# Optimization experiments

Hardware: AMD Instinct MI355X
Metric: run time of the kernel (lower is better)

Reference implementation:

```python
import jax, jax.numpy as jnp
import numpy as np

B, N, C, NSAMPLE = 4, 1024, 512, 32
RADIUS, HMIN, HMAX = 0.05, -0.02, 0.04
EPS = 1e-5


def setup_inputs() -> dict:
    key = jax.random.key(0)
    ks = jax.random.split(key, 6)
    # points in a ~20cm cube so the 5cm cylinder actually captures neighbors
    seed_xyz_graspable = jax.random.uniform(ks[0], (B, N, 3), jnp.float32) * 0.2
    seed_features_graspable = jax.random.normal(ks[1], (B, C, N), jnp.float32)
    rot_raw = jax.random.normal(ks[2], (B, N, 3, 3), jnp.float32)
    vp_rot, _ = jnp.linalg.qr(rot_raw)  # proper-ish per-seed view rotations
    W1 = jax.random.normal(ks[3], (512, 3 + C), jnp.float32) / np.float32(np.sqrt(3 + C))
    g1 = jnp.ones((512,), jnp.float32)
    b1 = jnp.zeros((512,), jnp.float32)
    W2 = jax.random.normal(ks[4], (512, 512), jnp.float32) / np.float32(np.sqrt(512))
    g2 = jnp.ones((512,), jnp.float32)
    b2 = jnp.zeros((512,), jnp.float32)
    return dict(seed_xyz_graspable=seed_xyz_graspable,
                seed_features_graspable=seed_features_graspable,
                vp_rot=vp_rot, W1=W1, g1=g1, b1=b1, W2=W2, g2=g2, b2=b2)


def _cylinder_query(xyz, rot):
    # offsets d[b,m,n] = xyz[b,n] - query[b,m], rotated into the cylinder frame (d @ R)
    d = xyz[:, None, :, :] - xyz[:, :, None, :]                 # (B,M,N,3)
    r = jnp.einsum('bmnd,bmde->bmne', d, rot)                   # (B,M,N,3)
    mask = (r[..., 1] ** 2 + r[..., 2] ** 2 < RADIUS ** 2) \
         & (r[..., 0] > HMIN) & (r[..., 0] < HMAX)              # (B,M,N)
    # first NSAMPLE valid indices; pad with the first valid index (CUDA kernel semantics)
    cand = jnp.where(mask, jnp.arange(N, dtype=jnp.int32)[None, None, :], N)
    idx = jnp.sort(cand, axis=-1)[..., :NSAMPLE]                # (B,M,S)
    idx = jnp.where(idx == N, idx[..., :1], idx)
    return idx


def _bn_relu(x, g, b):
    # training-mode BatchNorm2d over (B, M, S) per output channel; x: (B,O,M,S)
    mean = jnp.mean(x, axis=(0, 2, 3), keepdims=True)
    var = jnp.var(x, axis=(0, 2, 3), keepdims=True)
    xn = (x - mean) * jax.lax.rsqrt(var + EPS)
    return jax.nn.relu(xn * g[None, :, None, None] + b[None, :, None, None])


def reference(seed_xyz_graspable, seed_features_graspable, vp_rot, W1, g1, b1, W2, g2, b2):
    xyz = seed_xyz_graspable                                    # (B,N,3)
    idx = _cylinder_query(xyz, vp_rot)                          # (B,M,S) int32
    # gather neighbor coordinates and center/rotate/normalize
    grouped_xyz = jnp.take_along_axis(xyz[:, None], idx[..., None], axis=2)   # (B,M,S,3)
    local = grouped_xyz - xyz[:, :, None, :]
    local = jnp.einsum('bmsd,bmde->bmse', local, vp_rot) / RADIUS             # normalize_xyz
    # gather neighbor features
    feats = jnp.swapaxes(seed_features_graspable, 1, 2)                       # (B,N,C)
    gfeat = jnp.take_along_axis(feats[:, None], idx[..., None], axis=2)       # (B,M,S,C)
    x = jnp.concatenate([local, gfeat], axis=-1)                              # (B,M,S,3+C)
    # SharedMLP: 1x1 conv (no bias) + BN + ReLU, twice; channels-first layout (B,O,M,S)
    h = _bn_relu(jnp.einsum('bmsc,oc->boms', x, W1), g1, b1)
    h = _bn_relu(jnp.einsum('boms,po->bpms', h, W2), g2, b2)
    # max-pool over the nsample axis -> (B,512,M)
    return jnp.max(h, axis=-1)
```

## Files before the change

kernel.cpp:

```cpp
#include <hip/hip_runtime.h>
#include <hip/hip_bf16.h>
#include <stdint.h>

#define BATCH 4
#define NPTS  1024
#define CIN   512
#define NS    32
#define P_TOT (BATCH*NPTS*NS)
#define CO    512
#define RADIUS_F 0.05f
#define HMIN_F  (-0.02f)
#define HMAX_F  (0.04f)

typedef __attribute__((ext_vector_type(8))) short short8;
typedef __attribute__((ext_vector_type(4))) float f32x4;

__device__ __forceinline__ unsigned short f2bf(float f) {
  unsigned int x = __float_as_uint(f);
  x = x + 0x7fffu + ((x >> 16) & 1u);
  return (unsigned short)(x >> 16);
}
__device__ __forceinline__ float bf2f(unsigned short u) {
  return __uint_as_float(((unsigned int)u) << 16);
}
__device__ __forceinline__ unsigned int cvtpk(float lo, float hi) {
  unsigned int r;
  asm("v_cvt_pk_bf16_f32 %0, %1, %2" : "=v"(r) : "v"(lo), "v"(hi));
  return r;
}
__device__ __forceinline__ void load_lds16(const void* g, void* l) {
  __builtin_amdgcn_global_load_lds((const __attribute__((address_space(1))) void*)g,
                                   (__attribute__((address_space(3))) void*)l, 16, 0, 0);
}

__global__ void cyl_query_kernel(const float* __restrict__ xyz,
                                 const float* __restrict__ rot,
                                 int* __restrict__ idxout,
                                 float* __restrict__ lxyz) {
  int bm = blockIdx.x;
  int b = bm >> 10;
  int lane = threadIdx.x;
  const float* ctr = xyz + (size_t)bm * 3;
  float cx = ctr[0], cy = ctr[1], cz = ctr[2];
  const float* R = rot + (size_t)bm * 9;
  float r00=R[0],r01=R[1],r02=R[2],r10=R[3],r11=R[4],r12=R[5],r20=R[6],r21=R[7],r22=R[8];
  __shared__ int sidx[32];
  int taken = 0;
  for (int base = 0; base < NPTS && taken < NS; base += 64) {
    int n = base + lane;
    const float* p = xyz + ((size_t)b * NPTS + n) * 3;
    float dx = p[0]-cx, dy = p[1]-cy, dz = p[2]-cz;
    float rx = dx*r00 + dy*r10 + dz*r20;
    float ry = dx*r01 + dy*r11 + dz*r21;
    float rz = dx*r02 + dy*r12 + dz*r22;
    bool ok = (ry*ry + rz*rz < RADIUS_F*RADIUS_F) && (rx > HMIN_F) && (rx < HMAX_F);
    unsigned long long bal = __ballot(ok);
    if (ok) {
      int slot = taken + __popcll(bal & ((1ull << lane) - 1ull));
      if (slot < NS) sidx[slot] = n;
    }
    taken += __popcll(bal);
  }
  __syncthreads();
  int filled = taken < NS ? taken : NS;
  if (lane < NS) {
    int nsel = (lane < filled) ? sidx[lane] : sidx[0];
    size_t pp = (size_t)bm * NS + lane;
    idxout[pp] = nsel;
    const float* pn = xyz + ((size_t)b * NPTS + nsel) * 3;
    float dx = pn[0]-cx, dy = pn[1]-cy, dz = pn[2]-cz;
    const float inv = 1.0f / RADIUS_F;
    float rx = (dx*r00 + dy*r10 + dz*r20) * inv;
    float ry = (dx*r01 + dy*r11 + dz*r21) * inv;
    float rz = (dx*r02 + dy*r12 + dz*r22) * inv;
    float* lw = lxyz + pp * 3;
    lw[0] = rx; lw[1] = ry; lw[2] = rz;
  }
}

__global__ void transpose_feats(const float* __restrict__ feats,
                                unsigned short* __restrict__ featsT) {
  __shared__ float tile[64][65];
  int b = blockIdx.z, cb = blockIdx.y, nb = blockIdx.x;
  int t = threadIdx.x, tr = t >> 6, tc = t & 63;
  #pragma unroll
  for (int j = 0; j < 16; ++j) {
    int c = cb*64 + j*4 + tr;
    tile[j*4+tr][tc] = feats[((size_t)b*CIN + c)*NPTS + nb*64 + tc];
  }
  __syncthreads();
  #pragma unroll
  for (int j = 0; j < 16; ++j) {
    int n = nb*64 + j*4 + tr;
    featsT[((size_t)b*NPTS + n)*CIN + cb*64 + tc] = f2bf(tile[tc][j*4+tr]);
  }
}

__global__ void build_weights(const float* __restrict__ W1,
                              const float* __restrict__ W2,
                              unsigned short* __restrict__ w1f,
                              float* __restrict__ w1l,
                              unsigned short* __restrict__ w2b) {
  int i = blockIdx.x*256 + threadIdx.x;
  if (i < 512*512) {
    int o = i >> 9, k = i & 511;
    w1f[i] = f2bf(W1[o*515 + 3 + k]);
    w2b[i] = f2bf(W2[i]);
  }
  if (i < 512*3) {
    w1l[i] = W1[(i/3)*515 + (i%3)];
  }
}

__global__ __launch_bounds__(256) void scatter_kernel(
    const int* __restrict__ idx, const float* __restrict__ lxyz,
    float* __restrict__ L4, float* __restrict__ GM) {
  int i = blockIdx.x*256 + threadIdx.x;
  int b = i >> 15;
  int n = idx[i];
  const float* lw = lxyz + (size_t)i*3;
  float lx = lw[0], ly = lw[1], lz = lw[2];
  float* dst = L4 + (((size_t)b << 10) + n)*4;
  atomicAdd(dst+0, lx); atomicAdd(dst+1, ly);
  atomicAdd(dst+2, lz); atomicAdd(dst+3, 1.0f);
  float m[9] = {lx, ly, lz, lx*lx, lx*ly, lx*lz, ly*ly, ly*lz, lz*lz};
  #pragma unroll
  for (int d = 1; d < 64; d <<= 1)
    #pragma unroll
    for (int e = 0; e < 9; ++e) m[e] += __shfl_xor(m[e], d);
  __shared__ float mred[9];
  if (threadIdx.x < 9) mred[threadIdx.x] = 0.f;
  __syncthreads();
  if ((threadIdx.x & 63) == 0)
    #pragma unroll
    for (int e = 0; e < 9; ++e) atomicAdd(&mred[e], m[e]);
  __syncthreads();
  if (threadIdx.x < 9) atomicAdd(&GM[threadIdx.x], mred[threadIdx.x]);
}

__global__ __launch_bounds__(256) void gemm1u_kernel(
    const unsigned short* __restrict__ A,
    const unsigned short* __restrict__ Bw,
    float* __restrict__ C,
    const float* __restrict__ L4,
    const float* __restrict__ w1l,
    float* __restrict__ sums)
{
  __shared__ unsigned short As[128*32];
  __shared__ unsigned short Bs[128*32];
  int bx = blockIdx.x;
  int ob = bx & 3;
  size_t p0 = (size_t)(bx >> 2) * 128;
  int o0 = ob * 128;
  int t = threadIdx.x;
  int w = t >> 6, lane = t & 63;
  int wr = w >> 1, wc = w & 1;
  int l15 = lane & 15, l4 = lane >> 4;
  f32x4 acc[4][4];
  f32x4 zf = {0.f, 0.f, 0.f, 0.f};
  #pragma unroll
  for (int mi = 0; mi < 4; ++mi)
    #pragma unroll
    for (int ni = 0; ni < 4; ++ni) acc[mi][ni] = zf;

  int c0 = 2*w;
  int srow = lane >> 2;
  int scole = (lane & 3) * 8;

  const unsigned short* abase[2];
  const unsigned short* bbase[2];
  #pragma unroll
  for (int cc = 0; cc < 2; ++cc) {
    int row = 16*(c0+cc) + srow;
    abase[cc] = A + (p0 + row)*(size_t)512 + scole;
    bbase[cc] = Bw + (size_t)(o0 + row)*512 + scole;
  }

  for (int k0 = 0; k0 < 512; k0 += 32) {
    #pragma unroll
    for (int cc = 0; cc < 2; ++cc) {
      int c = c0 + cc;
      load_lds16(abase[cc] + k0, (char*)As + c*1024);
      load_lds16(bbase[cc] + k0, (char*)Bs + c*1024);
    }
    __syncthreads();
    short8 af[4], bfr[4];
    #pragma unroll
    for (int mi = 0; mi < 4; ++mi)
      af[mi] = *(const short8*)(As + (wr*64 + mi*16 + l15)*32 + l4*8);
    #pragma unroll
    for (int ni = 0; ni < 4; ++ni)
      bfr[ni] = *(const short8*)(Bs + (wc*64 + ni*16 + l15)*32 + l4*8);
    #pragma unroll
    for (int mi = 0; mi < 4; ++mi)
      #pragma unroll
      for (int ni = 0; ni < 4; ++ni)
        acc[mi][ni] = __builtin_amdgcn_mfma_f32_16x16x32_bf16(af[mi], bfr[ni], acc[mi][ni], 0, 0, 0);
    __syncthreads();
  }
  #pragma unroll
  for (int mi = 0; mi < 4; ++mi)
    #pragma unroll
    for (int ni = 0; ni < 4; ++ni)
      #pragma unroll
      for (int j = 0; j < 4; ++j) {
        size_t p = p0 + wr*64 + mi*16 + l4*4 + j;
        int o = o0 + wc*64 + ni*16 + l15;
        C[p*512 + o] = acc[mi][ni][j];
      }
  #pragma unroll
  for (int ni = 0; ni < 4; ++ni) {
    int c = o0 + wc*64 + ni*16 + l15;
    float wa = w1l[c*3], wb = w1l[c*3+1], wcc = w1l[c*3+2];
    float s = 0.f, q = 0.f;
    #pragma unroll
    for (int mi = 0; mi < 4; ++mi)
      #pragma unroll
      for (int j = 0; j < 4; ++j) {
        size_t p = p0 + wr*64 + mi*16 + l4*4 + j;
        float4 L = *(const float4*)(L4 + p*4);
        float h = acc[mi][ni][j];
        float lw = L.x*wa + L.y*wb + L.z*wcc;
        s += L.w*h;
        q += L.w*h*h + 2.f*h*lw;
      }
    s += __shfl_xor(s, 16); q += __shfl_xor(q, 16);
    s += __shfl_xor(s, 32); q += __shfl_xor(q, 32);
    if (l4 == 0) {
      atomicAdd(&sums[c], s);
      atomicAdd(&sums[512 + c], q);
    }
  }
}

__global__ void finalize1_kernel(const float* __restrict__ sums,
                                 const float* __restrict__ GM,
                                 const float* __restrict__ w1l,
                                 const float* __restrict__ g,
                                 const float* __restrict__ bia,
                                 float* __restrict__ ss,
                                 float* __restrict__ w1ls) {
  int c = blockIdx.x*256 + threadIdx.x;
  if (c >= 512) return;
  float w0 = w1l[c*3], w1 = w1l[c*3+1], w2 = w1l[c*3+2];
  float S = sums[c] + w0*GM[0] + w1*GM[1] + w2*GM[2];
  float Q = sums[512+c] + w0*w0*GM[3] + 2.f*w0*w1*GM[4] + 2.f*w0*w2*GM[5]
                        + w1*w1*GM[6] + 2.f*w1*w2*GM[7] + w2*w2*GM[8];
  const float invN = 1.f / (float)P_TOT;
  float mean = S * invN;
  float var  = Q * invN - mean*mean;
  float sc = g[c] * rsqrtf(var + 1e-5f);
  ss[c] = sc;
  ss[512+c] = bia[c] - mean*sc;
  w1ls[c]        = sc * w0;
  w1ls[512 + c]  = sc * w1;
  w1ls[1024 + c] = sc * w2;
}

__global__ __launch_bounds__(256) void fold_kernel(float* __restrict__ h1u,
                                                   const float* __restrict__ ss) {
  size_t i = ((size_t)blockIdx.x*256 + threadIdx.x) * 4;
  int c = (int)(i & 511);
  float4 v = *(float4*)(h1u + i);
  float4 sc = *(const float4*)(ss + c);
  float4 sh = *(const float4*)(ss + 512 + c);
  v.x = fmaf(v.x, sc.x, sh.x);
  v.y = fmaf(v.y, sc.y, sh.y);
  v.z = fmaf(v.z, sc.z, sh.z);
  v.w = fmaf(v.w, sc.w, sh.w);
  *(float4*)(h1u + i) = v;
}

__global__ __launch_bounds__(512) void gemm2_kernel(
    const float* __restrict__ h1u,
    const int* __restrict__ idx,
    const float* __restrict__ lxyz,
    const float* __restrict__ w1ls,
    const unsigned short* __restrict__ Bw,
    float* __restrict__ sums,
    float* __restrict__ pmax,
    float* __restrict__ pmin)
{
  __shared__ unsigned short As[128*32];
  __shared__ unsigned short Bs[256*32];
  __shared__ float wl[1536];
  int bx = blockIdx.x;
  int ob = bx & 1;
  size_t p0 = (size_t)(bx >> 1) * 128;
  int o0 = ob * 256;
  int t = threadIdx.x;
  int w = t >> 6, lane = t & 63;
  int wr = w >> 2;
  int wc = w & 3;
  int l15 = lane & 15, l4 = lane >> 4;
  f32x4 acc[4][4];
  f32x4 zf = {0.f, 0.f, 0.f, 0.f};
  #pragma unroll
  for (int mi = 0; mi < 4; ++mi)
    #pragma unroll
    for (int ni = 0; ni < 4; ++ni) acc[mi][ni] = zf;

  int sl = (lane & 3) ^ ((lane >> 3) & 3);
  int scole = (lane & 3) * 8;
  int cA = (l4 ^ ((l15 >> 1) & 3)) * 8;

  wl[t] = w1ls[t]; wl[512 + t] = w1ls[512 + t]; wl[1024 + t] = w1ls[1024 + t];

  int arow = 16*w + (lane >> 2);
  int awoff = arow*64 + sl*16;
  const float* hptr;
  float lxr, lyr, lzr;
  {
    size_t p = p0 + arow;
    int b = (int)(p >> 15);
    int n = idx[p];
    hptr = h1u + (((size_t)b << 10) + n)*512 + scole;
    const float* lwp = lxyz + p*3;
    lxr = lwp[0]; lyr = lwp[1]; lzr = lwp[2];
  }
  const unsigned short* bptr[2];
  #pragma unroll
  for (int cc = 0; cc < 2; ++cc) {
    int brow = 16*(2*w + cc) + (lane >> 2);
    bptr[cc] = Bw + (size_t)(o0 + brow)*CIN + sl*8;
  }

  float4 hv0 = *(const float4*)(hptr);
  float4 hv1 = *(const float4*)(hptr + 4);
  __syncthreads();

  for (int k0 = 0; k0 < CIN; k0 += 32) {
    #pragma unroll
    for (int cc = 0; cc < 2; ++cc)
      load_lds16(bptr[cc] + k0, (char*)Bs + (2*w + cc)*1024);
    int ch0 = k0 + scole;
    float4 xa = *(const float4*)(wl + ch0);
    float4 xb = *(const float4*)(wl + ch0 + 4);
    float4 ya = *(const float4*)(wl + 512 + ch0);
    float4 yb = *(const float4*)(wl + 512 + ch0 + 4);
    float4 za = *(const float4*)(wl + 1024 + ch0);
    float4 zb = *(const float4*)(wl + 1024 + ch0 + 4);
    float w0[8] = {xa.x,xa.y,xa.z,xa.w,xb.x,xb.y,xb.z,xb.w};
    float w1[8] = {ya.x,ya.y,ya.z,ya.w,yb.x,yb.y,yb.z,yb.w};
    float w2[8] = {za.x,za.y,za.z,za.w,zb.x,zb.y,zb.z,zb.w};
    {
      float fv[8] = {hv0.x, hv0.y, hv0.z, hv0.w, hv1.x, hv1.y, hv1.z, hv1.w};
      float gv[8];
      #pragma unroll
      for (int e = 0; e < 8; ++e)
        gv[e] = fmaxf(fv[e] + lxr*w0[e] + lyr*w1[e] + lzr*w2[e], 0.f);
      unsigned int rv[4];
      #pragma unroll
      for (int j = 0; j < 4; ++j) rv[j] = cvtpk(gv[2*j], gv[2*j+1]);
      *(uint4*)((char*)As + awoff) = make_uint4(rv[0], rv[1], rv[2], rv[3]);
    }
    if (k0 + 32 < CIN) {
      hv0 = *(const float4*)(hptr + k0 + 32);
      hv1 = *(const float4*)(hptr + k0 + 36);
    }
    __syncthreads();
    short8 af[4], bfr[4];
    #pragma unroll
    for (int mi = 0; mi < 4; ++mi)
      af[mi] = *(const short8*)(As + (wr*64 + mi*16 + l15)*32 + cA);
    #pragma unroll
    for (int ni = 0; ni < 4; ++ni)
      bfr[ni] = *(const short8*)(Bs + (wc*64 + ni*16 + l15)*32 + cA);
    #pragma unroll
    for (int mi = 0; mi < 4; ++mi)
      #pragma unroll
      for (int ni = 0; ni < 4; ++ni)
        acc[mi][ni] = __builtin_amdgcn_mfma_f32_16x16x32_bf16(af[mi], bfr[ni], acc[mi][ni], 0, 0, 0);
    __syncthreads();
  }

  #pragma unroll
  for (int ni = 0; ni < 4; ++ni) {
    float s = 0.f, q = 0.f;
    #pragma unroll
    for (int mi = 0; mi < 4; ++mi)
      #pragma unroll
      for (int j = 0; j < 4; ++j) { float v = acc[mi][ni][j]; s += v; q += v*v; }
    s += __shfl_xor(s, 16); q += __shfl_xor(q, 16);
    s += __shfl_xor(s, 32); q += __shfl_xor(q, 32);
    if (l4 == 0) {
      int c = o0 + wc*64 + ni*16 + l15;
      atomicAdd(&sums[c], s);
      atomicAdd(&sums[512 + c], q);
    }
  }
  #pragma unroll
  for (int ni = 0; ni < 4; ++ni) {
    #pragma unroll
    for (int h = 0; h < 2; ++h) {
      float mx = -3.4e38f, mn = 3.4e38f;
      #pragma unroll
      for (int mi = 2*h; mi < 2*h + 2; ++mi)
        #pragma unroll
        for (int j = 0; j < 4; ++j) {
          float v = acc[mi][ni][j];
          mx = fmaxf(mx, v); mn = fminf(mn, v);
        }
      mx = fmaxf(mx, __shfl_xor(mx, 16)); mn = fminf(mn, __shfl_xor(mn, 16));
      mx = fmaxf(mx, __shfl_xor(mx, 32)); mn = fminf(mn, __shfl_xor(mn, 32));
      if (l4 == 0) {
        size_t bm = (p0 >> 5) + 2*wr + h;
        int o = o0 + wc*64 + ni*16 + l15;
        pmax[bm*512 + o] = mx;
        pmin[bm*512 + o] = mn;
      }
    }
  }
}

__global__ void final_transpose(const float* __restrict__ pmax,
                                const float* __restrict__ pmin,
                                const float* __restrict__ sums,
                                const float* __restrict__ g,
                                const float* __restrict__ bia,
                                float* __restrict__ out) {
  __shared__ float tile[64][65];
  __shared__ float scl[64], shl[64];
  int b = blockIdx.z, ob = blockIdx.y, mb = blockIdx.x;
  int t = threadIdx.x, tr = t >> 6, tc = t & 63;
  if (t < 64) {
    int c = ob*64 + t;
    const float invN = 1.f / (float)P_TOT;
    float mean = sums[c] * invN;
    float var  = sums[512+c] * invN - mean*mean;
    float sc = g[c] * rsqrtf(var + 1e-5f);
    scl[t] = sc;
    shl[t] = bia[c] - mean*sc;
  }
  __syncthreads();
  #pragma unroll
  for (int j = 0; j < 16; ++j) {
    int m = mb*64 + j*4 + tr;
    float sc = scl[tc], sh = shl[tc];
    size_t pi = (((size_t)b << 10) + m)*512 + ob*64 + tc;
    float v = (sc >= 0.f) ? pmax[pi] : pmin[pi];
    tile[j*4+tr][tc] = fmaxf(fmaf(v, sc, sh), 0.f);
  }
  __syncthreads();
  #pragma unroll
  for (int j = 0; j < 16; ++j) {
    int o = ob*64 + j*4 + tr;
    out[((size_t)b*512 + o)*1024 + mb*64 + tc] = tile[tc][j*4+tr];
  }
}

extern "C" void kernel_launch(void* const* d_in, const int* in_sizes, int n_in,
                              void* d_out, int out_size, void* d_ws, size_t ws_size,
                              hipStream_t stream) {
  const float* xyz   = (const float*)d_in[0];
  const float* feats = (const float*)d_in[1];
  const float* rot   = (const float*)d_in[2];
  const float* W1    = (const float*)d_in[3];
  const float* g1    = (const float*)d_in[4];
  const float* b1    = (const float*)d_in[5];
  const float* W2    = (const float*)d_in[6];
  const float* g2    = (const float*)d_in[7];
  const float* b2    = (const float*)d_in[8];
  float* out = (float*)d_out;
  char* wsb = (char*)d_ws;

  const size_t OFF_IDX    = 0;
  const size_t OFF_LXYZ   = OFF_IDX    + (size_t)P_TOT*4;
  const size_t OFF_FEATST = OFF_LXYZ   + (size_t)P_TOT*3*4;
  const size_t OFF_W1F    = OFF_FEATST + (size_t)BATCH*NPTS*CIN*2;
  const size_t OFF_W1L    = OFF_W1F    + (size_t)CO*512*2;
  const size_t OFF_W1LS   = OFF_W1L    + 8192;
  const size_t OFF_W2B    = OFF_W1LS   + 8192;
  const size_t OFF_STATS  = OFF_W2B    + (size_t)CO*CIN*2;
  const size_t OFF_L4     = OFF_STATS  + 16384;
  const size_t OFF_GM     = OFF_L4     + 65536;
  const size_t OFF_H1U    = OFF_GM     + 4096;
  const size_t OFF_PMAX   = OFF_H1U    + (size_t)BATCH*NPTS*CO*4;
  const size_t OFF_PMIN   = OFF_PMAX   + (size_t)BATCH*NPTS*CO*4;
  const size_t WS_NEED    = OFF_PMIN   + (size_t)BATCH*NPTS*CO*4;

  if (ws_size < WS_NEED) return;

  int* idx             = (int*)(wsb + OFF_IDX);
  float* lxyz          = (float*)(wsb + OFF_LXYZ);
  unsigned short* fT   = (unsigned short*)(wsb + OFF_FEATST);
  unsigned short* w1f  = (unsigned short*)(wsb + OFF_W1F);
  float* w1l           = (float*)(wsb + OFF_W1L);
  float* w1ls          = (float*)(wsb + OFF_W1LS);
  unsigned short* w2b  = (unsigned short*)(wsb + OFF_W2B);
  float* stats         = (float*)(wsb + OFF_STATS);
  float* sums1 = stats;
  float* ss1   = stats + 1024;
  float* sums2 = stats + 2048;
  float* L4            = (float*)(wsb + OFF_L4);
  float* GM            = (float*)(wsb + OFF_GM);
  float* h1u           = (float*)(wsb + OFF_H1U);
  float* pmax          = (float*)(wsb + OFF_PMAX);
  float* pmin          = (float*)(wsb + OFF_PMIN);

  hipMemsetAsync(stats, 0, 16384 + 65536 + 4096, stream);

  transpose_feats<<<dim3(NPTS/64, CIN/64, BATCH), 256, 0, stream>>>(feats, fT);
  build_weights<<<(512*512 + 255)/256, 256, 0, stream>>>(W1, W2, w1f, w1l, w2b);
  cyl_query_kernel<<<BATCH*NPTS, 64, 0, stream>>>(xyz, rot, idx, lxyz);
  scatter_kernel<<<P_TOT/256, 256, 0, stream>>>(idx, lxyz, L4, GM);

  gemm1u_kernel<<<(BATCH*NPTS/128)*4, 256, 0, stream>>>(fT, w1f, h1u, L4, w1l, sums1);
  finalize1_kernel<<<2, 256, 0, stream>>>(sums1, GM, w1l, g1, b1, ss1, w1ls);
  fold_kernel<<<(BATCH*NPTS*CO/4)/256, 256, 0, stream>>>(h1u, ss1);

  gemm2_kernel<<<(P_TOT/128)*2, 512, 0, stream>>>(h1u, idx, lxyz, w1ls, w2b,
                                                  sums2, pmax, pmin);

  final_transpose<<<dim3(NPTS/64, CO/64, BATCH), 256, 0, stream>>>(pmax, pmin,
                                                                   sums2, g2, b2, out);
}
```

Baseline: 197.5 us.

## Merge preprocessing kernels into one launch and fuse BN finalize into fold

Transpose, weight conversion, cylinder query and neighbor scatter now run as one heterogeneous kernel whose block ranges do the different jobs. The scatter statistics are computed inside the query step, and the global moment sums are spread over 32 partial slots to reduce atomic contention. The BN1 finalize is folded into the fold kernel, so each block recomputes the per-channel scale and shift in LDS. This removes four kernel launches and the idx/lxyz re-read, at the cost of redundant finalize work in every fold block.

After: 196.7 us. No clear change (-0.4%).

```diff
diff --git a/kernel.cpp b/kernel.cpp
--- a/kernel.cpp
+++ b/kernel.cpp
@@ -33,109 +33,89 @@
                                    (__attribute__((address_space(3))) void*)l, 16, 0, 0);
 }
 
-__global__ void cyl_query_kernel(const float* __restrict__ xyz,
-                                 const float* __restrict__ rot,
-                                 int* __restrict__ idxout,
-                                 float* __restrict__ lxyz) {
-  int bm = blockIdx.x;
-  int b = bm >> 10;
-  int lane = threadIdx.x;
-  const float* ctr = xyz + (size_t)bm * 3;
-  float cx = ctr[0], cy = ctr[1], cz = ctr[2];
-  const float* R = rot + (size_t)bm * 9;
-  float r00=R[0],r01=R[1],r02=R[2],r10=R[3],r11=R[4],r12=R[5],r20=R[6],r21=R[7],r22=R[8];
-  __shared__ int sidx[32];
-  int taken = 0;
-  for (int base = 0; base < NPTS && taken < NS; base += 64) {
-    int n = base + lane;
-    const float* p = xyz + ((size_t)b * NPTS + n) * 3;
-    float dx = p[0]-cx, dy = p[1]-cy, dz = p[2]-cz;
-    float rx = dx*r00 + dy*r10 + dz*r20;
-    float ry = dx*r01 + dy*r11 + dz*r21;
-    float rz = dx*r02 + dy*r12 + dz*r22;
-    bool ok = (ry*ry + rz*rz < RADIUS_F*RADIUS_F) && (rx > HMIN_F) && (rx < HMAX_F);
-    unsigned long long bal = __ballot(ok);
-    if (ok) {
-      int slot = taken + __popcll(bal & ((1ull << lane) - 1ull));
-      if (slot < NS) sidx[slot] = n;
-    }
-    taken += __popcll(bal);
-  }
-  __syncthreads();
-  int filled = taken < NS ? taken : NS;
-  if (lane < NS) {
-    int nsel = (lane < filled) ? sidx[lane] : sidx[0];
-    size_t pp = (size_t)bm * NS + lane;
-    idxout[pp] = nsel;
-    const float* pn = xyz + ((size_t)b * NPTS + nsel) * 3;
-    float dx = pn[0]-cx, dy = pn[1]-cy, dz = pn[2]-cz;
-    const float inv = 1.0f / RADIUS_F;
-    float rx = (dx*r00 + dy*r10 + dz*r20) * inv;
-    float ry = (dx*r01 + dy*r11 + dz*r21) * inv;
-    float rz = (dx*r02 + dy*r12 + dz*r22) * inv;
-    float* lw = lxyz + pp * 3;
-    lw[0] = rx; lw[1] = ry; lw[2] = rz;
-  }
-}
-
-__global__ void transpose_feats(const float* __restrict__ feats,
-                                unsigned short* __restrict__ featsT) {
+__global__ __launch_bounds__(256) void pre_kernel(
+    const float* __restrict__ feats, const float* __restrict__ W1,
+    const float* __restrict__ W2, const float* __restrict__ xyz,
+    const float* __restrict__ rot,
+    unsigned short* __restrict__ featsT, unsigned short* __restrict__ w1f,
+    float* __restrict__ w1l, unsigned short* __restrict__ w2b,
+    int* __restrict__ idxout, float* __restrict__ lxyz,
+    float* __restrict__ L4, float* __restrict__ GMP) {
   __shared__ float tile[64][65];
-  int b = blockIdx.z, cb = blockIdx.y, nb = blockIdx.x;
-  int t = threadIdx.x, tr = t >> 6, tc = t & 63;
-  #pragma unroll
-  for (int j = 0; j < 16; ++j) {
-    int c = cb*64 + j*4 + tr;
-    tile[j*4+tr][tc] = feats[((size_t)b*CIN + c)*NPTS + nb*64 + tc];
-  }
-  __syncthreads();
-  #pragma unroll
-  for (int j = 0; j < 16; ++j) {
-    int n = nb*64 + j*4 + tr;
-    featsT[((size_t)b*NPTS + n)*CIN + cb*64 + tc] = f2bf(tile[tc][j*4+tr]);
-  }
-}
-
-__global__ void build_weights(const float* __restrict__ W1,
-                              const float* __restrict__ W2,
-                              unsigned short* __restrict__ w1f,
-                              float* __restrict__ w1l,
-                              unsigned short* __restrict__ w2b) {
-  int i = blockIdx.x*256 + threadIdx.x;
-  if (i < 512*512) {
+  __shared__ int sidx[4][32];
+  int bx = blockIdx.x;
+  int t = threadIdx.x;
+  if (bx < 512) {
+    int nb = bx & 15, cb = (bx >> 4) & 7, b = bx >> 7;
+    int tr = t >> 6, tc = t & 63;
+    #pragma unroll
+    for (int j = 0; j < 16; ++j) {
+      int c = cb*64 + j*4 + tr;
+      tile[j*4+tr][tc] = feats[((size_t)b*CIN + c)*NPTS + nb*64 + tc];
+    }
+    __syncthreads();
+    #pragma unroll
+    for (int j = 0; j < 16; ++j) {
+      int n = nb*64 + j*4 + tr;
+      featsT[((size_t)b*NPTS + n)*CIN + cb*64 + tc] = f2bf(tile[tc][j*4+tr]);
+    }
+  } else if (bx < 1536) {
+    int i = (bx - 512)*256 + t;
     int o = i >> 9, k = i & 511;
     w1f[i] = f2bf(W1[o*515 + 3 + k]);
     w2b[i] = f2bf(W2[i]);
-  }
-  if (i < 512*3) {
-    w1l[i] = W1[(i/3)*515 + (i%3)];
-  }
-}
-
-__global__ __launch_bounds__(256) void scatter_kernel(
-    const int* __restrict__ idx, const float* __restrict__ lxyz,
-    float* __restrict__ L4, float* __restrict__ GM) {
-  int i = blockIdx.x*256 + threadIdx.x;
-  int b = i >> 15;
-  int n = idx[i];
-  const float* lw = lxyz + (size_t)i*3;
-  float lx = lw[0], ly = lw[1], lz = lw[2];
-  float* dst = L4 + (((size_t)b << 10) + n)*4;
-  atomicAdd(dst+0, lx); atomicAdd(dst+1, ly);
-  atomicAdd(dst+2, lz); atomicAdd(dst+3, 1.0f);
-  float m[9] = {lx, ly, lz, lx*lx, lx*ly, lx*lz, ly*ly, ly*lz, lz*lz};
-  #pragma unroll
-  for (int d = 1; d < 64; d <<= 1)
-    #pragma unroll
-    for (int e = 0; e < 9; ++e) m[e] += __shfl_xor(m[e], d);
-  __shared__ float mred[9];
-  if (threadIdx.x < 9) mred[threadIdx.x] = 0.f;
-  __syncthreads();
-  if ((threadIdx.x & 63) == 0)
-    #pragma unroll
-    for (int e = 0; e < 9; ++e) atomicAdd(&mred[e], m[e]);
-  __syncthreads();
-  if (threadIdx.x < 9) atomicAdd(&GM[threadIdx.x], mred[threadIdx.x]);
+    if (i < 1536) w1l[i] = W1[(i/3)*515 + (i%3)];
+  } else {
+    int w = t >> 6, lane = t & 63;
+    int bm = (bx - 1536)*4 + w;
+    int b = bm >> 10;
+    const float* ctr = xyz + (size_t)bm * 3;
+    float cx = ctr[0], cy = ctr[1], cz = ctr[2];
+    const float* R = rot + (size_t)bm * 9;
+    float r00=R[0],r01=R[1],r02=R[2],r10=R[3],r11=R[4],r12=R[5],r20=R[6],r21=R[7],r22=R[8];
+    int taken = 0;
+    for (int base = 0; base < NPTS && taken < NS; base += 64) {
+      int n = base + lane;
+      const float* p = xyz + ((size_t)b * NPTS + n) * 3;
+      float dx = p[0]-cx, dy = p[1]-cy, dz = p[2]-cz;
+      float rx = dx*r00 + dy*r10 + dz*r20;
+      float ry = dx*r01 + dy*r11 + dz*r21;
+      float rz = dx*r02 + dy*r12 + dz*r22;
+      bool ok = (ry*ry + rz*rz < RADIUS_F*RADIUS_F) && (rx > HMIN_F) && (rx < HMAX_F);
+      unsigned long long bal = __ballot(ok);
+      if (ok) {
+        int slot = taken + __popcll(bal & ((1ull << lane) - 1ull));
+        if (slot < NS) sidx[w][slot] = n;
+      }
+      taken += __popcll(bal);
+    }
+    __syncthreads();
+    int filled = taken < NS ? taken : NS;
+    float m[9] = {0.f,0.f,0.f,0.f,0.f,0.f,0.f,0.f,0.f};
+    if (lane < NS) {
+      int nsel = (lane < filled) ? sidx[w][lane] : sidx[w][0];
+      size_t pp = (size_t)bm * NS + lane;
+      idxout[pp] = nsel;
+      const float* pn = xyz + ((size_t)b * NPTS + nsel) * 3;
+      float dx = pn[0]-cx, dy = pn[1]-cy, dz = pn[2]-cz;
+      const float inv = 1.0f / RADIUS_F;
+      float rx = (dx*r00 + dy*r10 + dz*r20) * inv;
+      float ry = (dx*r01 + dy*r11 + dz*r21) * inv;
+      float rz = (dx*r02 + dy*r12 + dz*r22) * inv;
+      float* lw = lxyz + pp * 3;
+      lw[0] = rx; lw[1] = ry; lw[2] = rz;
+      float* dst = L4 + (((size_t)b << 10) + nsel)*4;
+      atomicAdd(dst+0, rx); atomicAdd(dst+1, ry);
+      atomicAdd(dst+2, rz); atomicAdd(dst+3, 1.0f);
+      m[0]=rx; m[1]=ry; m[2]=rz;
+      m[3]=rx*rx; m[4]=rx*ry; m[5]=rx*rz; m[6]=ry*ry; m[7]=ry*rz; m[8]=rz*rz;
+    }
+    #pragma unroll
+    for (int d = 1; d < 64; d <<= 1)
+      #pragma unroll
+      for (int e = 0; e < 9; ++e) m[e] += __shfl_xor(m[e], d);
+    if (lane < 9) atomicAdd(&GMP[(bm & 31)*12 + lane], m[lane]);
+  }
 }
 
 __global__ __launch_bounds__(256) void gemm1u_kernel(
@@ -233,41 +213,50 @@
   }
 }
 
-__global__ void finalize1_kernel(const float* __restrict__ sums,
-                                 const float* __restrict__ GM,
-                                 const float* __restrict__ w1l,
-                                 const float* __restrict__ g,
-                                 const float* __restrict__ bia,
-                                 float* __restrict__ ss,
-                                 float* __restrict__ w1ls) {
-  int c = blockIdx.x*256 + threadIdx.x;
-  if (c >= 512) return;
-  float w0 = w1l[c*3], w1 = w1l[c*3+1], w2 = w1l[c*3+2];
-  float S = sums[c] + w0*GM[0] + w1*GM[1] + w2*GM[2];
-  float Q = sums[512+c] + w0*w0*GM[3] + 2.f*w0*w1*GM[4] + 2.f*w0*w2*GM[5]
-                        + w1*w1*GM[6] + 2.f*w1*w2*GM[7] + w2*w2*GM[8];
-  const float invN = 1.f / (float)P_TOT;
-  float mean = S * invN;
-  float var  = Q * invN - mean*mean;
-  float sc = g[c] * rsqrtf(var + 1e-5f);
-  ss[c] = sc;
-  ss[512+c] = bia[c] - mean*sc;
-  w1ls[c]        = sc * w0;
-  w1ls[512 + c]  = sc * w1;
-  w1ls[1024 + c] = sc * w2;
-}
-
-__global__ __launch_bounds__(256) void fold_kernel(float* __restrict__ h1u,
-                                                   const float* __restrict__ ss) {
-  size_t i = ((size_t)blockIdx.x*256 + threadIdx.x) * 4;
+__global__ __launch_bounds__(256) void fold_fin_kernel(
+    float* __restrict__ h1u,
+    const float* __restrict__ sums,
+    const float* __restrict__ GMP,
+    const float* __restrict__ w1l,
+    const float* __restrict__ g,
+    const float* __restrict__ bia,
+    float* __restrict__ w1ls) {
+  __shared__ float ssl[1024];
+  __shared__ float gms[9];
+  int t = threadIdx.x;
+  if (t < 9) {
+    float s = 0.f;
+    #pragma unroll
+    for (int k = 0; k < 32; ++k) s += GMP[k*12 + t];
+    gms[t] = s;
+  }
+  __syncthreads();
+  #pragma unroll
+  for (int cc = t; cc < 512; cc += 256) {
+    float w0 = w1l[cc*3], w1 = w1l[cc*3+1], w2 = w1l[cc*3+2];
+    float S = sums[cc] + w0*gms[0] + w1*gms[1] + w2*gms[2];
+    float Q = sums[512+cc] + w0*w0*gms[3] + 2.f*w0*w1*gms[4] + 2.f*w0*w2*gms[5]
+                           + w1*w1*gms[6] + 2.f*w1*w2*gms[7] + w2*w2*gms[8];
+    const float invN = 1.f / (float)P_TOT;
+    float mean = S * invN;
+    float var  = Q * invN - mean*mean;
+    float sc = g[cc] * rsqrtf(var + 1e-5f);
+    ssl[cc] = sc;
+    ssl[512+cc] = bia[cc] - mean*sc;
+    if (blockIdx.x == 0) {
+      w1ls[cc]        = sc * w0;
+      w1ls[512 + cc]  = sc * w1;
+      w1ls[1024 + cc] = sc * w2;
+    }
+  }
+  __syncthreads();
+  size_t i = ((size_t)blockIdx.x*256 + t) * 4;
   int c = (int)(i & 511);
   float4 v = *(float4*)(h1u + i);
-  float4 sc = *(const float4*)(ss + c);
-  float4 sh = *(const float4*)(ss + 512 + c);
-  v.x = fmaf(v.x, sc.x, sh.x);
-  v.y = fmaf(v.y, sc.y, sh.y);
-  v.z = fmaf(v.z, sc.z, sh.z);
-  v.w = fmaf(v.w, sc.w, sh.w);
+  v.x = fmaf(v.x, ssl[c],   ssl[512+c]);
+  v.y = fmaf(v.y, ssl[c+1], ssl[512+c+1]);
+  v.z = fmaf(v.z, ssl[c+2], ssl[512+c+2]);
+  v.w = fmaf(v.w, ssl[c+3], ssl[512+c+3]);
   *(float4*)(h1u + i) = v;
 }
 
@@ -473,8 +462,8 @@
   const size_t OFF_W2B    = OFF_W1LS   + 8192;
   const size_t OFF_STATS  = OFF_W2B    + (size_t)CO*CIN*2;
   const size_t OFF_L4     = OFF_STATS  + 16384;
-  const size_t OFF_GM     = OFF_L4     + 65536;
-  const size_t OFF_H1U    = OFF_GM     + 4096;
+  const size_t OFF_GMP    = OFF_L4     + 65536;
+  const size_t OFF_H1U    = OFF_GMP    + 4096;
   const size_t OFF_PMAX   = OFF_H1U    + (size_t)BATCH*NPTS*CO*4;
   const size_t OFF_PMIN   = OFF_PMAX   + (size_t)BATCH*NPTS*CO*4;
   const size_t WS_NEED    = OFF_PMIN   + (size_t)BATCH*NPTS*CO*4;
@@ -490,24 +479,22 @@
   unsigned short* w2b  = (unsigned short*)(wsb + OFF_W2B);
   float* stats         = (float*)(wsb + OFF_STATS);
   float* sums1 = stats;
-  float* ss1   = stats + 1024;
   float* sums2 = stats + 2048;
   float* L4            = (float*)(wsb + OFF_L4);
-  float* GM            = (float*)(wsb + OFF_GM);
+  float* GMP           = (float*)(wsb + OFF_GMP);
   float* h1u           = (float*)(wsb + OFF_H1U);
   float* pmax          = (float*)(wsb + OFF_PMAX);
   float* pmin          = (float*)(wsb + OFF_PMIN);
 
   hipMemsetAsync(stats, 0, 16384 + 65536 + 4096, stream);
 
-  transpose_feats<<<dim3(NPTS/64, CIN/64, BATCH), 256, 0, stream>>>(feats, fT);
-  build_weights<<<(512*512 + 255)/256, 256, 0, stream>>>(W1, W2, w1f, w1l, w2b);
-  cyl_query_kernel<<<BATCH*NPTS, 64, 0, stream>>>(xyz, rot, idx, lxyz);
-  scatter_kernel<<<P_TOT/256, 256, 0, stream>>>(idx, lxyz, L4, GM);
+  pre_kernel<<<2560, 256, 0, stream>>>(feats, W1, W2, xyz, rot,
+                                       fT, w1f, w1l, w2b, idx, lxyz, L4, GMP);
 
   gemm1u_kernel<<<(BATCH*NPTS/128)*4, 256, 0, stream>>>(fT, w1f, h1u, L4, w1l, sums1);
-  finalize1_kernel<<<2, 256, 0, stream>>>(sums1, GM, w1l, g1, b1, ss1, w1ls);
-  fold_kernel<<<(BATCH*NPTS*CO/4)/256, 256, 0, stream>>>(h1u, ss1);
+
+  fold_fin_kernel<<<(BATCH*NPTS*CO/4)/256, 256, 0, stream>>>(h1u, sums1, GMP,
+                                                             w1l, g1, b1, w1ls);
 
   gemm2_kernel<<<(P_TOT/128)*2, 512, 0, stream>>>(h1u, idx, lxyz, w1ls, w2b,
                                                   sums2, pmax, pmin);
```
